# Kernel tuning notes

Measured on AMD Instinct MI355X. Metric: run time of the kernel, lower is better.

## Reference

```python
import jax, jax.numpy as jnp
import numpy as np

THR = 1.0     # snntorch Leaky default threshold
BETA = 0.9    # args.beta
ALPHA = 2.0   # surrogate.atan default alpha

@jax.custom_vjp
def atan_spike(x):
    # Heaviside forward, arctan surrogate gradient (snntorch surrogate.atan)
    return (x > 0).astype(x.dtype)

def _aspk_fwd(x):
    return atan_spike(x), x

def _aspk_bwd(x, g):
    return (g * (ALPHA / 2.0) / (1.0 + (jnp.pi / 2.0 * ALPHA * x) ** 2),)

atan_spike.defvjp(_aspk_fwd, _aspk_bwd)

def setup_inputs() -> dict:
    key = jax.random.key(0)
    k = jax.random.split(key, 5)
    B, D, H, C = 32768, 187, 50, 5
    return {
        "x": jax.random.normal(k[0], (B, D), dtype=jnp.float32),
        "W1": jax.random.normal(k[1], (H, D), dtype=jnp.float32) * (1.0 / np.sqrt(D)),
        "b1": jax.random.normal(k[2], (H,), dtype=jnp.float32) * 0.01,
        "W2": jax.random.normal(k[3], (C, H), dtype=jnp.float32) * (1.0 / np.sqrt(H)),
        "b2": jax.random.normal(k[4], (C,), dtype=jnp.float32) * 0.01,
        "num_steps": 100,
    }

def reference(x, W1, b1, W2, b2, num_steps):
    B = x.shape[0]
    dt = x.dtype
    # fc1(x) is identical every timestep (x is static), compute once
    cur1 = x @ W1.T + b1  # [B, 50]

    def step(carry, _):
        mem1, mem2 = carry
        # Leaky: reset computed from PREVIOUS mem (detached), subtract mechanism
        reset1 = jax.lax.stop_gradient((mem1 > THR).astype(dt))
        mem1 = BETA * mem1 + cur1 - reset1 * THR
        spk1 = atan_spike(mem1 - THR)
        cur2 = spk1 @ W2.T + b2  # [B, num_classes]
        reset2 = jax.lax.stop_gradient((mem2 > THR).astype(dt))
        mem2 = BETA * mem2 + cur2 - reset2 * THR
        spk2 = atan_spike(mem2 - THR)
        return (mem1, mem2), (spk2, mem2)

    init = (jnp.zeros((B, W1.shape[0]), dt), jnp.zeros((B, W2.shape[0]), dt))
    _, (spk_rec, mem_rec) = jax.lax.scan(step, init, None, length=num_steps)
    return spk_rec, mem_rec  # each [num_steps, B, num_classes]
```

## Files before the change

### kernel.cpp

```cpp
#include <hip/hip_runtime.h>

typedef float v2f __attribute__((ext_vector_type(2)));
typedef float v4f __attribute__((ext_vector_type(4)));

#define DD   187
#define HH   50
#define PH   64
#define HPJ  14
#define HPL  16
#define NP   7
#define NC   5
#define RPB  64
#define BLK  256
#define DCH  64
#define NCHUNK 3
#define XSS  68
#define BETA 0.9f

__device__ __forceinline__ float dpp_xor1(float v) {
    return __builtin_bit_cast(float,
        __builtin_amdgcn_mov_dpp(__builtin_bit_cast(int, v), 0xB1, 0xF, 0xF, true));
}
__device__ __forceinline__ float dpp_xor2(float v) {
    return __builtin_bit_cast(float,
        __builtin_amdgcn_mov_dpp(__builtin_bit_cast(int, v), 0x4E, 0xF, 0xF, true));
}

__device__ __forceinline__ float spike1(float m) {
    float t = fmaf(m, 0x1.0p60f, -0x1.0p60f);
    return fminf(fmaxf(t, 0.f), 1.f);
}
__device__ __forceinline__ v2f spike2(v2f m) {
    const v2f BIG2  = { 0x1.0p60f,  0x1.0p60f};
    const v2f NBIG2 = {-0x1.0p60f, -0x1.0p60f};
    const v2f ONE2  = {1.f, 1.f};
    const v2f ZERO2 = {0.f, 0.f};
    v2f t = __builtin_elementwise_fma(m, BIG2, NBIG2);
    return __builtin_elementwise_min(__builtin_elementwise_max(t, ZERO2), ONE2);
}

__device__ __forceinline__ v2f vlo(v4f v) { return __builtin_shufflevector(v, v, 0, 1); }
__device__ __forceinline__ v2f vhi(v4f v) { return __builtin_shufflevector(v, v, 2, 3); }

__global__ __launch_bounds__(BLK) __attribute__((amdgpu_waves_per_eu(2, 2)))
void snn_kernel(const float* __restrict__ x,
                const float* __restrict__ W1,
                const float* __restrict__ b1,
                const float* __restrict__ W2,
                const float* __restrict__ b2,
                const int*   __restrict__ nsp,
                float* __restrict__ out, int Brows)
{
    __shared__ __align__(16) float xs[RPB * XSS];
    __shared__ __align__(16) float w1t[DCH * PH];

    const int tid = threadIdx.x;
    const int p   = tid >> 2;
    const int k   = tid & 3;
    const int row = blockIdx.x * RPB + p;
    const int NS  = nsp[0];

    v2f acc[NP];
#pragma unroll
    for (int i = 0; i < NP; ++i) acc[i] = (v2f){0.f, 0.f};

    for (int ch = 0; ch < NCHUNK; ++ch) {
        const int d0 = ch * DCH;
        for (int i = tid; i < RPB * DCH; i += BLK) {
            int r = i >> 6, dd = i & 63;
            int d = d0 + dd;
            xs[r * XSS + dd] = (d < DD) ? x[(size_t)(blockIdx.x * RPB + r) * DD + d] : 0.f;
        }
        for (int i = tid; i < DCH * PH; i += BLK) {
            int dd = i >> 6, s = i & 63;
            int kk = s >> 4, j = s & 15;
            int h = kk * HPJ + j;
            int d = d0 + dd;
            w1t[dd * PH + s] = (j < HPJ && h < HH && d < DD) ? W1[h * DD + d] : 0.f;
        }
        __syncthreads();

        const float* xr = xs + p * XSS;
#pragma unroll 2
        for (int d4 = 0; d4 < DCH / 4; ++d4) {
            v4f xv4 = *(const v4f*)(xr + 4 * d4);
#pragma unroll
            for (int j = 0; j < 4; ++j) {
                int d = 4 * d4 + j;
                const float* wbase = w1t + d * PH + k * HPL;
                v4f w0 = *(const v4f*)(wbase);
                v4f w1v = *(const v4f*)(wbase + 4);
                v4f w2v = *(const v4f*)(wbase + 8);
                v2f w3 = *(const v2f*)(wbase + 12);
                float xv = xv4[j];
                v2f xvv = {xv, xv};
                acc[0] = __builtin_elementwise_fma(xvv, vlo(w0),  acc[0]);
                acc[1] = __builtin_elementwise_fma(xvv, vhi(w0),  acc[1]);
                acc[2] = __builtin_elementwise_fma(xvv, vlo(w1v), acc[2]);
                acc[3] = __builtin_elementwise_fma(xvv, vhi(w1v), acc[3]);
                acc[4] = __builtin_elementwise_fma(xvv, vlo(w2v), acc[4]);
                acc[5] = __builtin_elementwise_fma(xvv, vhi(w2v), acc[5]);
                acc[6] = __builtin_elementwise_fma(xvv, w3,       acc[6]);
            }
        }
        __syncthreads();
    }

    v2f c1[NP];
#pragma unroll
    for (int i = 0; i < NP; ++i) {
        int h0 = k * HPJ + 2 * i;
        v2f bb;
        bb.x = (h0     < HH) ? b1[h0]     : 0.f;
        bb.y = (h0 + 1 < HH) ? b1[h0 + 1] : 0.f;
        c1[i] = acc[i] + bb;
    }
    if (k == 3) c1[6].y = 2.0f;

    v2f w2r[NC][NP];
#pragma unroll
    for (int c = 0; c < NC; ++c)
#pragma unroll
        for (int i = 0; i < NP; ++i) {
            int h0 = k * HPJ + 2 * i;
            w2r[c][i].x = (h0     < HH) ? W2[c * HH + h0]     : 0.f;
            w2r[c][i].y = (h0 + 1 < HH) ? W2[c * HH + h0 + 1] : 0.f;
        }
    if (k == 3) {
#pragma unroll
        for (int c = 0; c < NC; ++c) w2r[c][6].y = b2[c];
    }

    v2f m1[NP], s1[NP];
#pragma unroll
    for (int i = 0; i < NP; ++i) { m1[i] = (v2f){0.f, 0.f}; s1[i] = (v2f){0.f, 0.f}; }
    float mA = 0.f, sA = 0.f, mB = 0.f, sB = 0.f;

    const size_t stride = (size_t)Brows * NC;
    float* spkBase = out;
    float* memBase = out + (size_t)NS * stride;
    const int offA = row * NC + k;
    const int offB = row * NC + 4;
    const v2f BETA2 = {BETA, BETA};

    v2f cp[NC];
    auto S1 = [&]() {
#pragma unroll
        for (int c = 0; c < NC; ++c) cp[c] = (v2f){0.f, 0.f};
#pragma unroll
        for (int i = 0; i < NP; ++i) {
            v2f m = __builtin_elementwise_fma(BETA2, m1[i], c1[i]) - s1[i];
            m1[i] = m;
            v2f s = spike2(m);
            s1[i] = s;
#pragma unroll
            for (int c = 0; c < NC; ++c)
                cp[c] = __builtin_elementwise_fma(s, w2r[c][i], cp[c]);
        }
    };

    S1();
    for (int t = 0; t < NS; ++t) {
        float cur2[NC];
#pragma unroll
        for (int c = 0; c < NC; ++c) {
            float r = cp[c].x + cp[c].y;
            r += dpp_xor1(r);
            r += dpp_xor2(r);
            cur2[c] = r;
        }
        S1();

        float cA = (k == 1) ? cur2[1] : (k == 2) ? cur2[2] :
                   (k == 3) ? cur2[3] : cur2[0];
        float cB = cur2[4];

        mA = fmaf(BETA, mA, cA) - sA;
        sA = spike1(mA);
        mB = fmaf(BETA, mB, cB) - sB;
        sB = spike1(mB);

        spkBase[offA] = sA;
        memBase[offA] = mA;
        if (k == 0) { spkBase[offB] = sB; memBase[offB] = mB; }

        spkBase += stride;
        memBase += stride;
    }
}

extern "C" void kernel_launch(void* const* d_in, const int* in_sizes, int n_in,
                              void* d_out, int out_size, void* d_ws, size_t ws_size,
                              hipStream_t stream) {
    const float* x  = (const float*)d_in[0];
    const float* W1 = (const float*)d_in[1];
    const float* b1 = (const float*)d_in[2];
    const float* W2 = (const float*)d_in[3];
    const float* b2 = (const float*)d_in[4];
    const int*   ns = (const int*)d_in[5];
    int B = in_sizes[0] / DD;
    int nblocks = B / RPB;
    snn_kernel<<<nblocks, BLK, 0, stream>>>(x, W1, b1, W2, b2, ns, (float*)d_out, B);
}
```

Before: 223.2 us.

## Process two rows per thread group with half-size blocks and med3 spike clamp

Each 4-thread group now handles two batch rows instead of one, which halves the block to 128 threads and the x/W1 staging chunk to 32 columns. This lets the same W1 and W2 register values feed both rows, and it gives the recurrent loop two independent chains to interleave so latency is better hidden. The spike clamp now uses fmed3 instead of min/max. The cost is roughly double the register state per thread, occupancy forced to one wave per EU, and scattered stores that may coalesce differently.

Result: slower. 286.6 us (+28.4%).

```diff
diff --git a/kernel.cpp b/kernel.cpp
--- a/kernel.cpp
+++ b/kernel.cpp
@@ -11,10 +11,10 @@
 #define NP   7
 #define NC   5
 #define RPB  64
-#define BLK  256
-#define DCH  64
-#define NCHUNK 3
-#define XSS  68
+#define BLK  128
+#define DCH  32
+#define NCHUNK 6
+#define XSS  44
 #define BETA 0.9f
 
 __device__ __forceinline__ float dpp_xor1(float v) {
@@ -28,21 +28,22 @@
 
 __device__ __forceinline__ float spike1(float m) {
     float t = fmaf(m, 0x1.0p60f, -0x1.0p60f);
-    return fminf(fmaxf(t, 0.f), 1.f);
+    return __builtin_amdgcn_fmed3f(t, 0.f, 1.f);
 }
 __device__ __forceinline__ v2f spike2(v2f m) {
     const v2f BIG2  = { 0x1.0p60f,  0x1.0p60f};
     const v2f NBIG2 = {-0x1.0p60f, -0x1.0p60f};
-    const v2f ONE2  = {1.f, 1.f};
-    const v2f ZERO2 = {0.f, 0.f};
     v2f t = __builtin_elementwise_fma(m, BIG2, NBIG2);
-    return __builtin_elementwise_min(__builtin_elementwise_max(t, ZERO2), ONE2);
+    v2f s;
+    s.x = __builtin_amdgcn_fmed3f(t.x, 0.f, 1.f);
+    s.y = __builtin_amdgcn_fmed3f(t.y, 0.f, 1.f);
+    return s;
 }
 
 __device__ __forceinline__ v2f vlo(v4f v) { return __builtin_shufflevector(v, v, 0, 1); }
 __device__ __forceinline__ v2f vhi(v4f v) { return __builtin_shufflevector(v, v, 2, 3); }
 
-__global__ __launch_bounds__(BLK) __attribute__((amdgpu_waves_per_eu(2, 2)))
+__global__ __launch_bounds__(BLK, 1) __attribute__((amdgpu_waves_per_eu(1, 1)))
 void snn_kernel(const float* __restrict__ x,
                 const float* __restrict__ W1,
                 const float* __restrict__ b1,
@@ -54,20 +55,20 @@
     __shared__ __align__(16) float xs[RPB * XSS];
     __shared__ __align__(16) float w1t[DCH * PH];
 
-    const int tid = threadIdx.x;
-    const int p   = tid >> 2;
-    const int k   = tid & 3;
-    const int row = blockIdx.x * RPB + p;
-    const int NS  = nsp[0];
-
-    v2f acc[NP];
-#pragma unroll
-    for (int i = 0; i < NP; ++i) acc[i] = (v2f){0.f, 0.f};
+    const int tid  = threadIdx.x;
+    const int p    = tid >> 2;
+    const int k    = tid & 3;
+    const int row0 = blockIdx.x * RPB + 2 * p;
+    const int NS   = nsp[0];
+
+    v2f acca[NP], accb[NP];
+#pragma unroll
+    for (int i = 0; i < NP; ++i) { acca[i] = (v2f){0.f, 0.f}; accb[i] = (v2f){0.f, 0.f}; }
 
     for (int ch = 0; ch < NCHUNK; ++ch) {
         const int d0 = ch * DCH;
         for (int i = tid; i < RPB * DCH; i += BLK) {
-            int r = i >> 6, dd = i & 63;
+            int r = i >> 5, dd = i & 31;
             int d = d0 + dd;
             xs[r * XSS + dd] = (d < DD) ? x[(size_t)(blockIdx.x * RPB + r) * DD + d] : 0.f;
         }
@@ -80,10 +81,12 @@
         }
         __syncthreads();
 
-        const float* xr = xs + p * XSS;
+        const float* xr0 = xs + (2 * p)     * XSS;
+        const float* xr1 = xs + (2 * p + 1) * XSS;
 #pragma unroll 2
         for (int d4 = 0; d4 < DCH / 4; ++d4) {
-            v4f xv4 = *(const v4f*)(xr + 4 * d4);
+            v4f xa4 = *(const v4f*)(xr0 + 4 * d4);
+            v4f xb4 = *(const v4f*)(xr1 + 4 * d4);
 #pragma unroll
             for (int j = 0; j < 4; ++j) {
                 int d = 4 * d4 + j;
@@ -92,30 +95,38 @@
                 v4f w1v = *(const v4f*)(wbase + 4);
                 v4f w2v = *(const v4f*)(wbase + 8);
                 v2f w3 = *(const v2f*)(wbase + 12);
-                float xv = xv4[j];
-                v2f xvv = {xv, xv};
-                acc[0] = __builtin_elementwise_fma(xvv, vlo(w0),  acc[0]);
-                acc[1] = __builtin_elementwise_fma(xvv, vhi(w0),  acc[1]);
-                acc[2] = __builtin_elementwise_fma(xvv, vlo(w1v), acc[2]);
-                acc[3] = __builtin_elementwise_fma(xvv, vhi(w1v), acc[3]);
-                acc[4] = __builtin_elementwise_fma(xvv, vlo(w2v), acc[4]);
-                acc[5] = __builtin_elementwise_fma(xvv, vhi(w2v), acc[5]);
-                acc[6] = __builtin_elementwise_fma(xvv, w3,       acc[6]);
+                v2f xa = {xa4[j], xa4[j]};
+                v2f xb = {xb4[j], xb4[j]};
+                acca[0] = __builtin_elementwise_fma(xa, vlo(w0),  acca[0]);
+                accb[0] = __builtin_elementwise_fma(xb, vlo(w0),  accb[0]);
+                acca[1] = __builtin_elementwise_fma(xa, vhi(w0),  acca[1]);
+                accb[1] = __builtin_elementwise_fma(xb, vhi(w0),  accb[1]);
+                acca[2] = __builtin_elementwise_fma(xa, vlo(w1v), acca[2]);
+                accb[2] = __builtin_elementwise_fma(xb, vlo(w1v), accb[2]);
+                acca[3] = __builtin_elementwise_fma(xa, vhi(w1v), acca[3]);
+                accb[3] = __builtin_elementwise_fma(xb, vhi(w1v), accb[3]);
+                acca[4] = __builtin_elementwise_fma(xa, vlo(w2v), acca[4]);
+                accb[4] = __builtin_elementwise_fma(xb, vlo(w2v), accb[4]);
+                acca[5] = __builtin_elementwise_fma(xa, vhi(w2v), acca[5]);
+                accb[5] = __builtin_elementwise_fma(xb, vhi(w2v), accb[5]);
+                acca[6] = __builtin_elementwise_fma(xa, w3,       acca[6]);
+                accb[6] = __builtin_elementwise_fma(xb, w3,       accb[6]);
             }
         }
         __syncthreads();
     }
 
-    v2f c1[NP];
+    v2f c1a[NP], c1b[NP];
 #pragma unroll
     for (int i = 0; i < NP; ++i) {
         int h0 = k * HPJ + 2 * i;
         v2f bb;
         bb.x = (h0     < HH) ? b1[h0]     : 0.f;
         bb.y = (h0 + 1 < HH) ? b1[h0 + 1] : 0.f;
-        c1[i] = acc[i] + bb;
-    }
-    if (k == 3) c1[6].y = 2.0f;
+        c1a[i] = acca[i] + bb;
+        c1b[i] = accb[i] + bb;
+    }
+    if (k == 3) { c1a[6].y = 2.0f; c1b[6].y = 2.0f; }
 
     v2f w2r[NC][NP];
 #pragma unroll
@@ -131,58 +142,78 @@
         for (int c = 0; c < NC; ++c) w2r[c][6].y = b2[c];
     }
 
-    v2f m1[NP], s1[NP];
-#pragma unroll
-    for (int i = 0; i < NP; ++i) { m1[i] = (v2f){0.f, 0.f}; s1[i] = (v2f){0.f, 0.f}; }
-    float mA = 0.f, sA = 0.f, mB = 0.f, sB = 0.f;
+    v2f m1a[NP], s1a[NP], m1b[NP], s1b[NP];
+#pragma unroll
+    for (int i = 0; i < NP; ++i) {
+        m1a[i] = (v2f){0.f, 0.f}; s1a[i] = (v2f){0.f, 0.f};
+        m1b[i] = (v2f){0.f, 0.f}; s1b[i] = (v2f){0.f, 0.f};
+    }
+    float mA0 = 0.f, sA0 = 0.f, mB0 = 0.f, sB0 = 0.f;
+    float mA1 = 0.f, sA1 = 0.f, mB1 = 0.f, sB1 = 0.f;
 
     const size_t stride = (size_t)Brows * NC;
     float* spkBase = out;
     float* memBase = out + (size_t)NS * stride;
-    const int offA = row * NC + k;
-    const int offB = row * NC + 4;
+    const int offA0 = row0 * NC + k;
+    const int offA1 = offA0 + NC;
+    const int offB0 = row0 * NC + 4;
+    const int offB1 = offB0 + NC;
     const v2f BETA2 = {BETA, BETA};
-
-    v2f cp[NC];
+    const v2f ZERO2 = {0.f, 0.f};
+
+    v2f cpa[NC], cpb[NC];
     auto S1 = [&]() {
 #pragma unroll
-        for (int c = 0; c < NC; ++c) cp[c] = (v2f){0.f, 0.f};
+        for (int c = 0; c < NC; ++c) { cpa[c] = ZERO2; cpb[c] = ZERO2; }
 #pragma unroll
         for (int i = 0; i < NP; ++i) {
-            v2f m = __builtin_elementwise_fma(BETA2, m1[i], c1[i]) - s1[i];
-            m1[i] = m;
-            v2f s = spike2(m);
-            s1[i] = s;
-#pragma unroll
-            for (int c = 0; c < NC; ++c)
-                cp[c] = __builtin_elementwise_fma(s, w2r[c][i], cp[c]);
+            v2f ma = __builtin_elementwise_fma(BETA2, m1a[i], c1a[i]) - s1a[i];
+            v2f mb = __builtin_elementwise_fma(BETA2, m1b[i], c1b[i]) - s1b[i];
+            m1a[i] = ma; m1b[i] = mb;
+            v2f sa = spike2(ma);
+            v2f sb = spike2(mb);
+            s1a[i] = sa; s1b[i] = sb;
+#pragma unroll
+            for (int c = 0; c < NC; ++c) {
+                cpa[c] = __builtin_elementwise_fma(sa, w2r[c][i], cpa[c]);
+                cpb[c] = __builtin_elementwise_fma(sb, w2r[c][i], cpb[c]);
+            }
         }
     };
 
     S1();
     for (int t = 0; t < NS; ++t) {
-        float cur2[NC];
+        float cur2a[NC], cur2b[NC];
 #pragma unroll
         for (int c = 0; c < NC; ++c) {
-            float r = cp[c].x + cp[c].y;
-            r += dpp_xor1(r);
-            r += dpp_xor2(r);
-            cur2[c] = r;
+            float ra = cpa[c].x + cpa[c].y;
+            float rb = cpb[c].x + cpb[c].y;
+            ra += dpp_xor1(ra);  rb += dpp_xor1(rb);
+            ra += dpp_xor2(ra);  rb += dpp_xor2(rb);
+            cur2a[c] = ra; cur2b[c] = rb;
         }
         S1();
 
-        float cA = (k == 1) ? cur2[1] : (k == 2) ? cur2[2] :
-                   (k == 3) ? cur2[3] : cur2[0];
-        float cB = cur2[4];
-
-        mA = fmaf(BETA, mA, cA) - sA;
-        sA = spike1(mA);
-        mB = fmaf(BETA, mB, cB) - sB;
-        sB = spike1(mB);
-
-        spkBase[offA] = sA;
-        memBase[offA] = mA;
-        if (k == 0) { spkBase[offB] = sB; memBase[offB] = mB; }
+        float cA0 = (k == 1) ? cur2a[1] : (k == 2) ? cur2a[2] :
+                    (k == 3) ? cur2a[3] : cur2a[0];
+        float cA1 = (k == 1) ? cur2b[1] : (k == 2) ? cur2b[2] :
+                    (k == 3) ? cur2b[3] : cur2b[0];
+        float cB0 = cur2a[4];
+        float cB1 = cur2b[4];
+
+        mA0 = fmaf(BETA, mA0, cA0) - sA0;  sA0 = spike1(mA0);
+        mA1 = fmaf(BETA, mA1, cA1) - sA1;  sA1 = spike1(mA1);
+        mB0 = fmaf(BETA, mB0, cB0) - sB0;  sB0 = spike1(mB0);
+        mB1 = fmaf(BETA, mB1, cB1) - sB1;  sB1 = spike1(mB1);
+
+        spkBase[offA0] = sA0;
+        spkBase[offA1] = sA1;
+        memBase[offA0] = mA0;
+        memBase[offA1] = mA1;
+        if (k == 0) {
+            spkBase[offB0] = sB0;  spkBase[offB1] = sB1;
+            memBase[offB0] = mB0;  memBase[offB1] = mB1;
+        }
 
         spkBase += stride;
         memBase += stride;
```
